# Performance work log

Hardware: AMD Instinct MI355X
Metric: run time of the kernel (lower is better)

## Reference

```python
import jax, jax.numpy as jnp
import numpy as np

B, T, C = 4, 2048, 768
H, KVH, D = 6, 6, 128
HALF = D // 2


def setup_inputs() -> dict:
    key = jax.random.key(0)
    ks = jax.random.split(key, 5)
    x = jax.random.normal(ks[0], (B, T, C), dtype=jnp.float32)
    # true rotary frequencies
    inv_freq = 1.0 / (10000.0 ** (jnp.arange(HALF, dtype=jnp.float32) / HALF))
    ang = jnp.arange(T, dtype=jnp.float32)[:, None] * inv_freq[None, :]  # [T, HALF]
    cos, sin = jnp.cos(ang), jnp.sin(ang)
    s = 0.02
    wq = jax.random.normal(ks[1], (H * D, C), dtype=jnp.float32) * s
    wk = jax.random.normal(ks[2], (KVH * D, C), dtype=jnp.float32) * s
    wv = jax.random.normal(ks[3], (KVH * D, C), dtype=jnp.float32) * s
    wproj = jax.random.normal(ks[4], (C, C), dtype=jnp.float32) * s
    return {"x": x, "cos": cos, "sin": sin, "wq": wq, "wk": wk, "wv": wv, "wproj": wproj}


def _norm(t, eps=1e-6):
    # torch: (x - mean) / (std + eps), std unbiased (ddof=1)
    mean = jnp.mean(t, axis=-1, keepdims=True)
    var = jnp.sum((t - mean) ** 2, axis=-1, keepdims=True) / (t.shape[-1] - 1)
    return (t - mean) / (jnp.sqrt(var) + eps)


def _rope(t, cos, sin):
    # t: [B, T, heads, D]; cos/sin: [T, HALF]
    x1, x2 = t[..., :HALF], t[..., HALF:]
    c = cos[None, :, None, :]
    s = sin[None, :, None, :]
    return jnp.concatenate([x1 * c + x2 * s, -x1 * s + x2 * c], axis=-1)


def reference(x, cos, sin, wq, wk, wv, wproj):
    q = jnp.einsum('btc,oc->bto', x, wq).reshape(B, T, H, D)
    k = jnp.einsum('btc,oc->bto', x, wk).reshape(B, T, KVH, D)
    v = jnp.einsum('btc,oc->bto', x, wv).reshape(B, T, KVH, D)
    q = _norm(_rope(q, cos, sin))
    k = _norm(_rope(k, cos, sin))
    # -> [B, heads, T, D]
    q = q.transpose(0, 2, 1, 3)
    k = k.transpose(0, 2, 1, 3)
    v = v.transpose(0, 2, 1, 3)
    # nrep = H // KVH == 1, repeat_kv is a no-op here
    scale = 1.0 / jnp.sqrt(jnp.float32(D))
    scores = jnp.einsum('bhtd,bhsd->bhts', q, k) * scale  # [B,H,T,T]
    causal = jnp.tril(jnp.ones((T, T), dtype=bool))
    scores = jnp.where(causal[None, None], scores, jnp.float32(-1e30))
    attn = jax.nn.softmax(scores, axis=-1)
    y = jnp.einsum('bhts,bhsd->bhtd', attn, v)
    y = y.transpose(0, 2, 1, 3).reshape(B, T, H * D)
    return jnp.einsum('bto,co->btc', y, wproj)
```

## Files before the change

### kernel.cpp

```cpp
#include <hip/hip_runtime.h>

#define BB 4
#define TT 2048
#define CC 768
#define HH 6
#define DD 128
#define BT (BB * TT)
#define HALF 64
#define NBH (BB * HH)
#define QKSCALE 0.12753785627919282f

typedef __bf16 v8bf __attribute__((ext_vector_type(8)));
typedef float f32x4 __attribute__((ext_vector_type(4)));

__device__ __forceinline__ unsigned short f2b(float f) {
  union { float f; unsigned u; } v; v.f = f;
  unsigned r = v.u + 0x7FFFu + ((v.u >> 16) & 1u);
  return (unsigned short)(r >> 16);
}
__device__ __forceinline__ float b2f(unsigned short u) {
  union { unsigned u; float f; } v; v.u = (unsigned)u << 16;
  return v.f;
}
__device__ __forceinline__ unsigned pk2(float f0, float f1) {
  union { float f; unsigned u; } a, b; a.f = f1; b.f = f0;
  return __builtin_amdgcn_perm(a.u, b.u, 0x07060302u);
}

__device__ __forceinline__ void load_lds16(const void* g, void* l) {
  __builtin_amdgcn_global_load_lds(
      (const __attribute__((address_space(1))) unsigned int*)g,
      (__attribute__((address_space(3))) unsigned int*)(unsigned int)(unsigned long long)(l),
      16, 0, 0);
}

__global__ __launch_bounds__(256) void cvt_all_kernel(const float* __restrict__ x,
                                                      const float* __restrict__ w0,
                                                      const float* __restrict__ w1,
                                                      const float* __restrict__ w2,
                                                      const float* __restrict__ w3,
                                                      unsigned short* __restrict__ xb,
                                                      unsigned short* __restrict__ wb) {
  int bx = blockIdx.x;
  const float* src;
  unsigned short* dst;
  int i;
  if (bx < 6144) {
    src = x; dst = xb; i = bx * 256 + threadIdx.x;
  } else {
    int bsel = (bx - 6144) / 576;
    src = bsel == 0 ? w0 : bsel == 1 ? w1 : bsel == 2 ? w2 : w3;
    dst = wb + bsel * 589824;
    i = ((bx - 6144) % 576) * 256 + threadIdx.x;
  }
  float4 f = ((const float4*)src)[i];
  ushort4 o;
  o.x = f2b(f.x); o.y = f2b(f.y); o.z = f2b(f.z); o.w = f2b(f.w);
  ((ushort4*)dst)[i] = o;
}

__global__ __launch_bounds__(256) void gemm_qkv(const unsigned short* __restrict__ A,
                                                const unsigned short* __restrict__ Wall,
                                                unsigned short* __restrict__ qb,
                                                unsigned short* __restrict__ kb,
                                                unsigned short* __restrict__ vt) {
  __shared__ __align__(16) unsigned short As[2][512 * 8];
  __shared__ __align__(16) unsigned short Bs[2][512 * 8];
  const int m0 = blockIdx.x * 128;
  const int wsel = blockIdx.y / HH, h = blockIdx.y % HH;
  const unsigned short* W = Wall + (size_t)wsel * 589824 + (size_t)h * 128 * CC;
  const int tid = threadIdx.x;
  const int wave = tid >> 6, lane = tid & 63;
  const int fr = lane & 15, quad = lane >> 4;
  const int wm = (wave & 1) * 64, wn = (wave >> 1) * 64;

  f32x4 acc[4][4];
#pragma unroll
  for (int i = 0; i < 4; i++)
#pragma unroll
    for (int j = 0; j < 4; j++) acc[i][j] = (f32x4){0.f, 0.f, 0.f, 0.f};

  auto stage = [&](int kk, int buf) {
#pragma unroll
    for (int it = 0; it < 2; it++) {
      int base_slot = wave * 128 + it * 64;
      int sigma = base_slot + lane;
      int r = sigma >> 2, g = (sigma & 3) ^ ((r >> 1) & 3);
      load_lds16(A + (size_t)(m0 + r) * CC + kk + g * 8, &As[buf][base_slot * 8]);
      load_lds16(W + (size_t)r * CC + kk + g * 8, &Bs[buf][base_slot * 8]);
    }
  };

  stage(0, 0);
  __syncthreads();
  for (int step = 0; step < CC / 32; step++) {
    int buf = step & 1;
    if (step + 1 < CC / 32) stage((step + 1) * 32, buf ^ 1);
    v8bf af[4], bfr[4];
#pragma unroll
    for (int i = 0; i < 4; i++) {
      int ra = wm + i * 16 + fr;
      af[i] = *(const v8bf*)&As[buf][(4 * ra + (quad ^ ((ra >> 1) & 3))) * 8];
      int rb = wn + i * 16 + fr;
      bfr[i] = *(const v8bf*)&Bs[buf][(4 * rb + (quad ^ ((rb >> 1) & 3))) * 8];
    }
#pragma unroll
    for (int i = 0; i < 4; i++)
#pragma unroll
      for (int j = 0; j < 4; j++)
        acc[i][j] = __builtin_amdgcn_mfma_f32_16x16x32_bf16(af[i], bfr[j], acc[i][j], 0, 0, 0);
    __syncthreads();
  }

  if (wsel < 2) {
    unsigned short* dst = wsel ? kb : qb;
#pragma unroll
    for (int i = 0; i < 4; i++) {
      int rr0 = m0 + wm + i * 16 + quad * 4;
      int b = rr0 >> 11, t0 = rr0 & 2047;
      size_t base = ((size_t)(b * HH + h) * TT + t0) * DD;
#pragma unroll
      for (int j = 0; j < 4; j++) {
        int d = wn + j * 16 + fr;
#pragma unroll
        for (int r = 0; r < 4; r++)
          dst[base + (size_t)r * DD + d] = f2b(acc[i][j][r]);
      }
    }
  } else {
#pragma unroll
    for (int i = 0; i < 4; i++) {
      int rr0 = m0 + wm + i * 16 + quad * 4;
      int b = rr0 >> 11, t0 = rr0 & 2047;
      int bh = b * HH + h;
#pragma unroll
      for (int j = 0; j < 4; j++) {
        int d = wn + j * 16 + fr;
        ushort4 u = { f2b(acc[i][j][0]), f2b(acc[i][j][1]),
                      f2b(acc[i][j][2]), f2b(acc[i][j][3]) };
        *(ushort4*)&vt[((size_t)bh * DD + d) * TT + t0] = u;
      }
    }
  }
}

__global__ __launch_bounds__(256) void gemm_w64(const unsigned short* __restrict__ A,
                                                const unsigned short* __restrict__ W,
                                                float* __restrict__ C) {
  __shared__ __align__(16) unsigned short As[2][256 * 8];
  __shared__ __align__(16) unsigned short Bs[2][512 * 8];
  const int m0 = blockIdx.x * 64, n0 = blockIdx.y * 128;
  const int tid = threadIdx.x;
  const int wave = tid >> 6, lane = tid & 63;
  const int fr = lane & 15, quad = lane >> 4;
  const int wm = (wave & 1) * 32, wn = (wave >> 1) * 64;

  f32x4 acc[2][4];
#pragma unroll
  for (int i = 0; i < 2; i++)
#pragma unroll
    for (int j = 0; j < 4; j++) acc[i][j] = (f32x4){0.f, 0.f, 0.f, 0.f};

  auto stage = [&](int kk, int buf) {
    {
      int base_slot = wave * 64;
      int sigma = base_slot + lane;
      int r = sigma >> 2, g = (sigma & 3) ^ ((r >> 1) & 3);
      load_lds16(A + (size_t)(m0 + r) * CC + kk + g * 8, &As[buf][base_slot * 8]);
    }
#pragma unroll
    for (int it = 0; it < 2; it++) {
      int base_slot = wave * 128 + it * 64;
      int sigma = base_slot + lane;
      int r = sigma >> 2, g = (sigma & 3) ^ ((r >> 1) & 3);
      load_lds16(W + (size_t)(n0 + r) * CC + kk + g * 8, &Bs[buf][base_slot * 8]);
    }
  };

  stage(0, 0);
  __syncthreads();
  for (int step = 0; step < CC / 32; step++) {
    int buf = step & 1;
    if (step + 1 < CC / 32) stage((step + 1) * 32, buf ^ 1);
    v8bf af[2], bfr[4];
#pragma unroll
    for (int i = 0; i < 2; i++) {
      int ra = wm + i * 16 + fr;
      af[i] = *(const v8bf*)&As[buf][(4 * ra + (quad ^ ((ra >> 1) & 3))) * 8];
    }
#pragma unroll
    for (int j = 0; j < 4; j++) {
      int rb = wn + j * 16 + fr;
      bfr[j] = *(const v8bf*)&Bs[buf][(4 * rb + (quad ^ ((rb >> 1) & 3))) * 8];
    }
#pragma unroll
    for (int i = 0; i < 2; i++)
#pragma unroll
      for (int j = 0; j < 4; j++)
        acc[i][j] = __builtin_amdgcn_mfma_f32_16x16x32_bf16(af[i], bfr[j], acc[i][j], 0, 0, 0);
    __syncthreads();
  }

  const int orow = m0 + wm + quad * 4;
#pragma unroll
  for (int i = 0; i < 2; i++)
#pragma unroll
    for (int j = 0; j < 4; j++) {
      int oc = n0 + wn + j * 16 + fr;
#pragma unroll
      for (int r = 0; r < 4; r++)
        C[(size_t)(orow + i * 16 + r) * CC + oc] = acc[i][j][r];
    }
}

__global__ __launch_bounds__(256) void rope_all_kernel(unsigned short* __restrict__ qb,
                                                       unsigned short* __restrict__ kb,
                                                       const float* __restrict__ cosb,
                                                       const float* __restrict__ sinb) {
  int bx = blockIdx.x;
  unsigned short* qk = (bx < 12288) ? qb : kb;
  float scale = (bx < 12288) ? QKSCALE : 1.0f;
  int idx = (bx % 12288) * 4 + (threadIdx.x >> 6);
  int lane = threadIdx.x & 63;
  int tpos = idx & (TT - 1);
  size_t base = (size_t)idx * DD;

  float x1 = b2f(qk[base + lane]);
  float x2 = b2f(qk[base + HALF + lane]);
  float c = cosb[tpos * HALF + lane];
  float s = sinb[tpos * HALF + lane];
  float o1 = x1 * c + x2 * s;
  float o2 = x2 * c - x1 * s;

  float sum = o1 + o2;
#pragma unroll
  for (int off = 32; off; off >>= 1) sum += __shfl_xor(sum, off);
  float mean = sum * (1.f / 128.f);
  float d1 = o1 - mean, d2 = o2 - mean;
  float vs = d1 * d1 + d2 * d2;
#pragma unroll
  for (int off = 32; off; off >>= 1) vs += __shfl_xor(vs, off);
  float inv = scale / (sqrtf(vs * (1.f / 127.f)) + 1e-6f);

  qk[base + lane] = f2b(d1 * inv);
  qk[base + HALF + lane] = f2b(d2 * inv);
}

__global__ __launch_bounds__(256, 4) void attn_mfma(const unsigned short* __restrict__ qtb,
                                                    const unsigned short* __restrict__ ktb,
                                                    const unsigned short* __restrict__ vtb,
                                                    unsigned short* __restrict__ Opart,
                                                    float* __restrict__ lpart) {
  __shared__ __align__(16) unsigned short Ks[2][512 * 8];
  __shared__ __align__(16) unsigned short Vts[2][512 * 8];

  const int u = blockIdx.x;
  const int bh = u % NBH;
  const int uu = u / NBH;
  int qt, c;
  if (uu < 16)      { qt = 15 - (uu >> 2); c = uu & 3; }
  else if (uu < 28) { int k = uu - 16; int q3 = k / 3; qt = 11 - q3; c = k - q3 * 3; }
  else if (uu < 36) { int k = uu - 28; qt = 7 - (k >> 1); c = k & 1; }
  else              { qt = 3 - (uu - 36); c = 0; }
  const int t0 = c * 16;
  const int t1 = min(t0 + 16, 4 * qt + 4);
  const int niter = t1 - t0;

  const int tid = threadIdx.x;
  const int wave = tid >> 6, lane = tid & 63;
  const int fr = lane & 15, quad = lane >> 4;
  const int idxf = 4 * ((quad & 1) * 32 + fr);
  const int idxs = idxf + 64;
  const size_t head_base = (size_t)bh * TT * DD;
  const int m0 = qt * 128 + wave * 32;

  v8bf qf[2][4];
#pragma unroll
  for (int qs = 0; qs < 2; qs++)
#pragma unroll
    for (int kbk = 0; kbk < 4; kbk++)
      qf[qs][kbk] = *(const v8bf*)(qtb + head_base +
                                   (size_t)(m0 + qs * 16 + fr) * DD + kbk * 32 + quad * 8);

  const __bf16 one_bf = (__bf16)1.0f;
  v8bf ones = {one_bf, one_bf, one_bf, one_bf, one_bf, one_bf, one_bf, one_bf};

  f32x4 oacc[2][8];
#pragma unroll
  for (int qs = 0; qs < 2; qs++)
#pragma unroll
    for (int i = 0; i < 8; i++) oacc[qs][i] = (f32x4){0.f, 0.f, 0.f, 0.f};
  f32x4 lacc[2] = {(f32x4){0.f, 0.f, 0.f, 0.f}, (f32x4){0.f, 0.f, 0.f, 0.f}};

  auto stage = [&](int jt, int buf) {
    const unsigned short* kbase = ktb + head_base + (size_t)(jt * 32) * DD;
    const unsigned short* vbase = vtb + head_base + jt * 32;
#pragma unroll
    for (int it = 0; it < 2; it++) {
      int base_slot = it * 256 + wave * 64;
      int sigma = base_slot + lane;
      int s = sigma >> 4, gk = (sigma & 15) ^ (s & 7);
      load_lds16(kbase + (size_t)s * DD + gk * 8, &Ks[buf][base_slot * 8]);
      int d = sigma >> 2, gv = (sigma & 3) ^ ((d >> 1) & 3);
      load_lds16(vbase + (size_t)d * TT + gv * 8, &Vts[buf][base_slot * 8]);
    }
  };

  stage(t0, 0);
  __syncthreads();

  for (int it = 0; it < niter; it++) {
    const int jt = t0 + it;
    const int buf = it & 1;
    if (it + 1 < niter) stage(jt + 1, buf ^ 1);

    const int j0 = jt * 32;
    if (j0 <= m0 + 31) {
      f32x4 st[2][2];
#pragma unroll
      for (int qs = 0; qs < 2; qs++) { st[qs][0] = (f32x4){0,0,0,0}; st[qs][1] = (f32x4){0,0,0,0}; }
      __builtin_amdgcn_s_setprio(1);
#pragma unroll
      for (int kbk = 0; kbk < 4; kbk++) {
        int g = 4 * kbk + quad;
        v8bf a0 = *(const v8bf*)&Ks[buf][(16 * fr + (g ^ (fr & 7))) * 8];
        v8bf a1 = *(const v8bf*)&Ks[buf][(16 * (fr + 16) + (g ^ (fr & 7))) * 8];
        st[0][0] = __builtin_amdgcn_mfma_f32_16x16x32_bf16(a0, qf[0][kbk], st[0][0], 0, 0, 0);
        st[0][1] = __builtin_amdgcn_mfma_f32_16x16x32_bf16(a1, qf[0][kbk], st[0][1], 0, 0, 0);
        st[1][0] = __builtin_amdgcn_mfma_f32_16x16x32_bf16(a0, qf[1][kbk], st[1][0], 0, 0, 0);
        st[1][1] = __builtin_amdgcn_mfma_f32_16x16x32_bf16(a1, qf[1][kbk], st[1][1], 0, 0, 0);
      }
      __builtin_amdgcn_s_setprio(0);

      const bool diag = (j0 + 31 > m0);
      v8bf pa0, pa1;
#pragma unroll
      for (int qs = 0; qs < 2; qs++) {
        float p[8];
        if (diag) {
          const int qrow = m0 + qs * 16 + fr;
#pragma unroll
          for (int r = 0; r < 4; r++) {
            int c0 = j0 + quad * 4 + r;
            p[r]     = (c0      <= qrow) ? exp2f(st[qs][0][r]) : 0.f;
            p[4 + r] = (c0 + 16 <= qrow) ? exp2f(st[qs][1][r]) : 0.f;
          }
        } else {
#pragma unroll
          for (int r = 0; r < 4; r++) { p[r] = exp2f(st[qs][0][r]); p[4 + r] = exp2f(st[qs][1][r]); }
        }
        unsigned A0 = pk2(p[0], p[1]), A1 = pk2(p[2], p[3]);
        unsigned B0 = pk2(p[4], p[5]), B1 = pk2(p[6], p[7]);
        unsigned alo0 = (unsigned)__builtin_amdgcn_ds_bpermute(idxf, (int)A0);
        unsigned alo1 = (unsigned)__builtin_amdgcn_ds_bpermute(idxf, (int)A1);
        unsigned ahi0 = (unsigned)__builtin_amdgcn_ds_bpermute(idxs, (int)A0);
        unsigned ahi1 = (unsigned)__builtin_amdgcn_ds_bpermute(idxs, (int)A1);
        unsigned blo0 = (unsigned)__builtin_amdgcn_ds_bpermute(idxf, (int)B0);
        unsigned blo1 = (unsigned)__builtin_amdgcn_ds_bpermute(idxf, (int)B1);
        unsigned bhi0 = (unsigned)__builtin_amdgcn_ds_bpermute(idxs, (int)B0);
        unsigned bhi1 = (unsigned)__builtin_amdgcn_ds_bpermute(idxs, (int)B1);
        const bool ql = (quad < 2);
        union { unsigned w[4]; v8bf v; } pa;
        pa.w[0] = ql ? alo0 : blo0;
        pa.w[1] = ql ? alo1 : blo1;
        pa.w[2] = ql ? ahi0 : bhi0;
        pa.w[3] = ql ? ahi1 : bhi1;
        if (qs == 0) pa0 = pa.v; else pa1 = pa.v;
      }

      __builtin_amdgcn_s_setprio(1);
#pragma unroll
      for (int nt2 = 0; nt2 < 8; nt2++) {
        int d = nt2 * 16 + fr;
        v8bf vb = *(const v8bf*)&Vts[buf][(4 * d + (quad ^ ((d >> 1) & 3))) * 8];
        oacc[0][nt2] = __builtin_amdgcn_mfma_f32_16x16x32_bf16(pa0, vb, oacc[0][nt2], 0, 0, 0);
        oacc[1][nt2] = __builtin_amdgcn_mfma_f32_16x16x32_bf16(pa1, vb, oacc[1][nt2], 0, 0, 0);
      }
      lacc[0] = __builtin_amdgcn_mfma_f32_16x16x32_bf16(pa0, ones, lacc[0], 0, 0, 0);
      lacc[1] = __builtin_amdgcn_mfma_f32_16x16x32_bf16(pa1, ones, lacc[1], 0, 0, 0);
      __builtin_amdgcn_s_setprio(0);
    }
    __syncthreads();
  }

  unsigned short* Oc = Opart + (size_t)c * (NBH * TT * DD) + head_base;
#pragma unroll
  for (int qs = 0; qs < 2; qs++) {
#pragma unroll
    for (int nt2 = 0; nt2 < 8; nt2++)
#pragma unroll
      for (int r = 0; r < 4; r++)
        Oc[(size_t)(m0 + qs * 16 + quad * 4 + r) * DD + nt2 * 16 + fr] = f2b(oacc[qs][nt2][r]);
    if (fr == 0) {
#pragma unroll
      for (int r = 0; r < 4; r++)
        lpart[c * (NBH * TT) + bh * TT + m0 + qs * 16 + quad * 4 + r] = lacc[qs][r];
    }
  }
}

__global__ __launch_bounds__(256) void combine_kernel(const unsigned short* __restrict__ Opart,
                                                      const float* __restrict__ lpart,
                                                      unsigned short* __restrict__ yb) {
  int idx = blockIdx.x * 256 + threadIdx.x;
  int row = idx >> 5;
  int dg = (idx & 31) * 4;
  int t = row & 2047;
  int qt = t >> 7;
  int nc = (4 * qt + 4 + 15) >> 4;

  float a0 = 0.f, a1 = 0.f, a2 = 0.f, a3 = 0.f, l = 0.f;
  for (int cchunk = 0; cchunk < nc; cchunk++) {
    ushort4 o = *(const ushort4*)&Opart[(size_t)cchunk * (NBH * TT * DD) + (size_t)row * DD + dg];
    a0 += b2f(o.x); a1 += b2f(o.y); a2 += b2f(o.z); a3 += b2f(o.w);
    l += lpart[cchunk * (NBH * TT) + row];
  }
  float linv = 1.f / l;
  int bh = row >> 11;
  int b = bh / HH, h = bh % HH;
  ushort4 uo = { f2b(a0 * linv), f2b(a1 * linv), f2b(a2 * linv), f2b(a3 * linv) };
  *(ushort4*)&yb[((size_t)(b * TT + t)) * CC + h * DD + dg] = uo;
}

extern "C" void kernel_launch(void* const* d_in, const int* in_sizes, int n_in,
                              void* d_out, int out_size, void* d_ws, size_t ws_size,
                              hipStream_t stream) {
  const float* x     = (const float*)d_in[0];
  const float* cosb  = (const float*)d_in[1];
  const float* sinb  = (const float*)d_in[2];
  const float* wq    = (const float*)d_in[3];
  const float* wk    = (const float*)d_in[4];
  const float* wv    = (const float*)d_in[5];
  const float* wproj = (const float*)d_in[6];
  float* out = (float*)d_out;

  char* w = (char*)d_ws;
  unsigned short* q_t   = (unsigned short*)(w);
  unsigned short* k_t   = (unsigned short*)(w + 12582912);
  unsigned short* v_t   = (unsigned short*)(w + 25165824);
  unsigned short* yb    = (unsigned short*)(w + 37748736);
  unsigned short* xb    = (unsigned short*)(w + 50331648);
  float*          lpart = (float*)(w + 50331648);
  unsigned short* wb    = (unsigned short*)(w + 62914560);
  unsigned short* Opart = (unsigned short*)(w + 67633152);

  cvt_all_kernel<<<8448, 256, 0, stream>>>(x, wq, wk, wv, wproj, xb, wb);

  gemm_qkv<<<dim3(BT / 128, 3 * HH), 256, 0, stream>>>(xb, wb, q_t, k_t, v_t);

  rope_all_kernel<<<24576, 256, 0, stream>>>(q_t, k_t, cosb, sinb);

  attn_mfma<<<960, 256, 0, stream>>>(q_t, k_t, v_t, Opart, lpart);
  combine_kernel<<<6144, 256, 0, stream>>>(Opart, lpart, yb);

  gemm_w64<<<dim3(BT / 64, CC / 128), 256, 0, stream>>>(yb, wb + 3 * 589824, out);
}
```

Baseline: 288.5 us.

## Double KV tile to 64 keys per iteration in MFMA attention kernel

Increases the per-iteration key/value tile from 32 to 64 keys, doubling LDS buffers and restructuring the staging swizzle, score MFMAs, masking, and PV accumulation for two k-slices. The aim is to halve the number of loop iterations and __syncthreads barriers per block and amortize per-iteration overhead. In exchange, LDS use doubles to 64KB and register pressure rises, and the min-4-blocks launch bound is dropped, which may lower occupancy. More work on the causal diagonal is also wasted because the masked tile is coarser.

```diff
diff --git a/kernel.cpp b/kernel.cpp
--- a/kernel.cpp
+++ b/kernel.cpp
@@ -246,13 +246,13 @@
   qk[base + HALF + lane] = f2b(d2 * inv);
 }
 
-__global__ __launch_bounds__(256, 4) void attn_mfma(const unsigned short* __restrict__ qtb,
-                                                    const unsigned short* __restrict__ ktb,
-                                                    const unsigned short* __restrict__ vtb,
-                                                    unsigned short* __restrict__ Opart,
-                                                    float* __restrict__ lpart) {
-  __shared__ __align__(16) unsigned short Ks[2][512 * 8];
-  __shared__ __align__(16) unsigned short Vts[2][512 * 8];
+__global__ __launch_bounds__(256) void attn_mfma(const unsigned short* __restrict__ qtb,
+                                                 const unsigned short* __restrict__ ktb,
+                                                 const unsigned short* __restrict__ vtb,
+                                                 unsigned short* __restrict__ Opart,
+                                                 float* __restrict__ lpart) {
+  __shared__ __align__(16) unsigned short Ks[2][1024 * 8];
+  __shared__ __align__(16) unsigned short Vts[2][1024 * 8];
 
   const int u = blockIdx.x;
   const int bh = u % NBH;
@@ -262,8 +262,8 @@
   else if (uu < 28) { int k = uu - 16; int q3 = k / 3; qt = 11 - q3; c = k - q3 * 3; }
   else if (uu < 36) { int k = uu - 28; qt = 7 - (k >> 1); c = k & 1; }
   else              { qt = 3 - (uu - 36); c = 0; }
-  const int t0 = c * 16;
-  const int t1 = min(t0 + 16, 4 * qt + 4);
+  const int t0 = c * 8;
+  const int t1 = min(t0 + 8, 2 * qt + 2);
   const int niter = t1 - t0;
 
   const int tid = threadIdx.x;
@@ -293,15 +293,15 @@
   f32x4 lacc[2] = {(f32x4){0.f, 0.f, 0.f, 0.f}, (f32x4){0.f, 0.f, 0.f, 0.f}};
 
   auto stage = [&](int jt, int buf) {
-    const unsigned short* kbase = ktb + head_base + (size_t)(jt * 32) * DD;
-    const unsigned short* vbase = vtb + head_base + jt * 32;
-#pragma unroll
-    for (int it = 0; it < 2; it++) {
+    const unsigned short* kbase = ktb + head_base + (size_t)(jt * 64) * DD;
+    const unsigned short* vbase = vtb + head_base + jt * 64;
+#pragma unroll
+    for (int it = 0; it < 4; it++) {
       int base_slot = it * 256 + wave * 64;
       int sigma = base_slot + lane;
       int s = sigma >> 4, gk = (sigma & 15) ^ (s & 7);
       load_lds16(kbase + (size_t)s * DD + gk * 8, &Ks[buf][base_slot * 8]);
-      int d = sigma >> 2, gv = (sigma & 3) ^ ((d >> 1) & 3);
+      int d = sigma >> 3, gv = (sigma & 7) ^ ((d >> 1) & 7);
       load_lds16(vbase + (size_t)d * TT + gv * 8, &Vts[buf][base_slot * 8]);
     }
   };
@@ -314,70 +314,89 @@
     const int buf = it & 1;
     if (it + 1 < niter) stage(jt + 1, buf ^ 1);
 
-    const int j0 = jt * 32;
+    const int j0 = jt * 64;
     if (j0 <= m0 + 31) {
-      f32x4 st[2][2];
-#pragma unroll
-      for (int qs = 0; qs < 2; qs++) { st[qs][0] = (f32x4){0,0,0,0}; st[qs][1] = (f32x4){0,0,0,0}; }
+      f32x4 st[2][4];
+#pragma unroll
+      for (int qs = 0; qs < 2; qs++)
+#pragma unroll
+        for (int sb = 0; sb < 4; sb++) st[qs][sb] = (f32x4){0.f, 0.f, 0.f, 0.f};
       __builtin_amdgcn_s_setprio(1);
 #pragma unroll
       for (int kbk = 0; kbk < 4; kbk++) {
         int g = 4 * kbk + quad;
-        v8bf a0 = *(const v8bf*)&Ks[buf][(16 * fr + (g ^ (fr & 7))) * 8];
-        v8bf a1 = *(const v8bf*)&Ks[buf][(16 * (fr + 16) + (g ^ (fr & 7))) * 8];
+        int gx = (g ^ (fr & 7)) * 8;
+        v8bf a0 = *(const v8bf*)&Ks[buf][(16 * fr) * 8 + gx];
+        v8bf a1 = *(const v8bf*)&Ks[buf][(16 * (fr + 16)) * 8 + gx];
+        v8bf a2 = *(const v8bf*)&Ks[buf][(16 * (fr + 32)) * 8 + gx];
+        v8bf a3 = *(const v8bf*)&Ks[buf][(16 * (fr + 48)) * 8 + gx];
         st[0][0] = __builtin_amdgcn_mfma_f32_16x16x32_bf16(a0, qf[0][kbk], st[0][0], 0, 0, 0);
         st[0][1] = __builtin_amdgcn_mfma_f32_16x16x32_bf16(a1, qf[0][kbk], st[0][1], 0, 0, 0);
+        st[0][2] = __builtin_amdgcn_mfma_f32_16x16x32_bf16(a2, qf[0][kbk], st[0][2], 0, 0, 0);
+        st[0][3] = __builtin_amdgcn_mfma_f32_16x16x32_bf16(a3, qf[0][kbk], st[0][3], 0, 0, 0);
         st[1][0] = __builtin_amdgcn_mfma_f32_16x16x32_bf16(a0, qf[1][kbk], st[1][0], 0, 0, 0);
         st[1][1] = __builtin_amdgcn_mfma_f32_16x16x32_bf16(a1, qf[1][kbk], st[1][1], 0, 0, 0);
+        st[1][2] = __builtin_amdgcn_mfma_f32_16x16x32_bf16(a2, qf[1][kbk], st[1][2], 0, 0, 0);
+        st[1][3] = __builtin_amdgcn_mfma_f32_16x16x32_bf16(a3, qf[1][kbk], st[1][3], 0, 0, 0);
       }
       __builtin_amdgcn_s_setprio(0);
 
-      const bool diag = (j0 + 31 > m0);
-      v8bf pa0, pa1;
+      const bool diag = (j0 + 63 > m0);
+      v8bf pa[2][2];
 #pragma unroll
       for (int qs = 0; qs < 2; qs++) {
-        float p[8];
+        float p[16];
         if (diag) {
           const int qrow = m0 + qs * 16 + fr;
 #pragma unroll
-          for (int r = 0; r < 4; r++) {
-            int c0 = j0 + quad * 4 + r;
-            p[r]     = (c0      <= qrow) ? exp2f(st[qs][0][r]) : 0.f;
-            p[4 + r] = (c0 + 16 <= qrow) ? exp2f(st[qs][1][r]) : 0.f;
-          }
+          for (int sb = 0; sb < 4; sb++)
+#pragma unroll
+            for (int r = 0; r < 4; r++) {
+              int c0 = j0 + sb * 16 + quad * 4 + r;
+              p[sb * 4 + r] = (c0 <= qrow) ? exp2f(st[qs][sb][r]) : 0.f;
+            }
         } else {
 #pragma unroll
-          for (int r = 0; r < 4; r++) { p[r] = exp2f(st[qs][0][r]); p[4 + r] = exp2f(st[qs][1][r]); }
+          for (int sb = 0; sb < 4; sb++)
+#pragma unroll
+            for (int r = 0; r < 4; r++) p[sb * 4 + r] = exp2f(st[qs][sb][r]);
         }
-        unsigned A0 = pk2(p[0], p[1]), A1 = pk2(p[2], p[3]);
-        unsigned B0 = pk2(p[4], p[5]), B1 = pk2(p[6], p[7]);
-        unsigned alo0 = (unsigned)__builtin_amdgcn_ds_bpermute(idxf, (int)A0);
-        unsigned alo1 = (unsigned)__builtin_amdgcn_ds_bpermute(idxf, (int)A1);
-        unsigned ahi0 = (unsigned)__builtin_amdgcn_ds_bpermute(idxs, (int)A0);
-        unsigned ahi1 = (unsigned)__builtin_amdgcn_ds_bpermute(idxs, (int)A1);
-        unsigned blo0 = (unsigned)__builtin_amdgcn_ds_bpermute(idxf, (int)B0);
-        unsigned blo1 = (unsigned)__builtin_amdgcn_ds_bpermute(idxf, (int)B1);
-        unsigned bhi0 = (unsigned)__builtin_amdgcn_ds_bpermute(idxs, (int)B0);
-        unsigned bhi1 = (unsigned)__builtin_amdgcn_ds_bpermute(idxs, (int)B1);
-        const bool ql = (quad < 2);
-        union { unsigned w[4]; v8bf v; } pa;
-        pa.w[0] = ql ? alo0 : blo0;
-        pa.w[1] = ql ? alo1 : blo1;
-        pa.w[2] = ql ? ahi0 : bhi0;
-        pa.w[3] = ql ? ahi1 : bhi1;
-        if (qs == 0) pa0 = pa.v; else pa1 = pa.v;
+#pragma unroll
+        for (int ks = 0; ks < 2; ks++) {
+          unsigned A0 = pk2(p[ks * 8 + 0], p[ks * 8 + 1]), A1 = pk2(p[ks * 8 + 2], p[ks * 8 + 3]);
+          unsigned B0 = pk2(p[ks * 8 + 4], p[ks * 8 + 5]), B1 = pk2(p[ks * 8 + 6], p[ks * 8 + 7]);
+          unsigned alo0 = (unsigned)__builtin_amdgcn_ds_bpermute(idxf, (int)A0);
+          unsigned alo1 = (unsigned)__builtin_amdgcn_ds_bpermute(idxf, (int)A1);
+          unsigned ahi0 = (unsigned)__builtin_amdgcn_ds_bpermute(idxs, (int)A0);
+          unsigned ahi1 = (unsigned)__builtin_amdgcn_ds_bpermute(idxs, (int)A1);
+          unsigned blo0 = (unsigned)__builtin_amdgcn_ds_bpermute(idxf, (int)B0);
+          unsigned blo1 = (unsigned)__builtin_amdgcn_ds_bpermute(idxf, (int)B1);
+          unsigned bhi0 = (unsigned)__builtin_amdgcn_ds_bpermute(idxs, (int)B0);
+          unsigned bhi1 = (unsigned)__builtin_amdgcn_ds_bpermute(idxs, (int)B1);
+          const bool ql = (quad < 2);
+          union { unsigned w[4]; v8bf v; } pw;
+          pw.w[0] = ql ? alo0 : blo0;
+          pw.w[1] = ql ? alo1 : blo1;
+          pw.w[2] = ql ? ahi0 : bhi0;
+          pw.w[3] = ql ? ahi1 : bhi1;
+          pa[qs][ks] = pw.v;
+        }
       }
 
       __builtin_amdgcn_s_setprio(1);
 #pragma unroll
-      for (int nt2 = 0; nt2 < 8; nt2++) {
-        int d = nt2 * 16 + fr;
-        v8bf vb = *(const v8bf*)&Vts[buf][(4 * d + (quad ^ ((d >> 1) & 3))) * 8];
-        oacc[0][nt2] = __builtin_amdgcn_mfma_f32_16x16x32_bf16(pa0, vb, oacc[0][nt2], 0, 0, 0);
-        oacc[1][nt2] = __builtin_amdgcn_mfma_f32_16x16x32_bf16(pa1, vb, oacc[1][nt2], 0, 0, 0);
+      for (int ks = 0; ks < 2; ks++) {
+#pragma unroll
+        for (int nt2 = 0; nt2 < 8; nt2++) {
+          int d = nt2 * 16 + fr;
+          int swz = (d >> 1) & 7;
+          v8bf vb = *(const v8bf*)&Vts[buf][(8 * d + ((quad + 4 * ks) ^ swz)) * 8];
+          oacc[0][nt2] = __builtin_amdgcn_mfma_f32_16x16x32_bf16(pa[0][ks], vb, oacc[0][nt2], 0, 0, 0);
+          oacc[1][nt2] = __builtin_amdgcn_mfma_f32_16x16x32_bf16(pa[1][ks], vb, oacc[1][nt2], 0, 0, 0);
+        }
+        lacc[0] = __builtin_amdgcn_mfma_f32_16x16x32_bf16(pa[0][ks], ones, lacc[0], 0, 0, 0);
+        lacc[1] = __builtin_amdgcn_mfma_f32_16x16x32_bf16(pa[1][ks], ones, lacc[1], 0, 0, 0);
       }
-      lacc[0] = __builtin_amdgcn_mfma_f32_16x16x32_bf16(pa0, ones, lacc[0], 0, 0, 0);
-      lacc[1] = __builtin_amdgcn_mfma_f32_16x16x32_bf16(pa1, ones, lacc[1], 0, 0, 0);
       __builtin_amdgcn_s_setprio(0);
     }
     __syncthreads();
```

After: 267.0 us. 7.5% less time.

## Halve attention query tile to 64 rows and rebalance block-to-chunk schedule

Applied to the files above, without the earlier changes.

The attention kernel now processes 64 query rows per block (16 per wave) instead of 128, which doubles the grid and uses a new longest-first mapping of blocks to key chunks. Each wave holds one Q fragment and one set of output accumulators, so register pressure drops and more blocks can be resident. The intent is better load balance and occupancy on the causal triangle. In exchange, every K/V tile staged into shared memory now feeds half as many query rows, which doubles K/V traffic and the staging and sync cost per unit of work.

```diff
diff --git a/kernel.cpp b/kernel.cpp
--- a/kernel.cpp
+++ b/kernel.cpp
@@ -246,24 +246,25 @@
   qk[base + HALF + lane] = f2b(d2 * inv);
 }
 
-__global__ __launch_bounds__(256, 4) void attn_mfma(const unsigned short* __restrict__ qtb,
-                                                    const unsigned short* __restrict__ ktb,
-                                                    const unsigned short* __restrict__ vtb,
-                                                    unsigned short* __restrict__ Opart,
-                                                    float* __restrict__ lpart) {
+__global__ __launch_bounds__(256) void attn_mfma(const unsigned short* __restrict__ qtb,
+                                                 const unsigned short* __restrict__ ktb,
+                                                 const unsigned short* __restrict__ vtb,
+                                                 unsigned short* __restrict__ Opart,
+                                                 float* __restrict__ lpart) {
   __shared__ __align__(16) unsigned short Ks[2][512 * 8];
   __shared__ __align__(16) unsigned short Vts[2][512 * 8];
 
   const int u = blockIdx.x;
   const int bh = u % NBH;
   const int uu = u / NBH;
-  int qt, c;
-  if (uu < 16)      { qt = 15 - (uu >> 2); c = uu & 3; }
-  else if (uu < 28) { int k = uu - 16; int q3 = k / 3; qt = 11 - q3; c = k - q3 * 3; }
-  else if (uu < 36) { int k = uu - 28; qt = 7 - (k >> 1); c = k & 1; }
-  else              { qt = 3 - (uu - 36); c = 0; }
+  int qb, c;
+  if (uu < 25)       { c = 0; qb = 31 - uu; }
+  else if (uu < 42)  { c = 1; qb = 31 - (uu - 25); }
+  else if (uu < 51)  { c = 2; qb = 31 - (uu - 42); }
+  else if (uu == 51) { c = 3; qb = 31; }
+  else { int uu2 = uu - 52; int sidx = uu2 >> 2; c = uu2 & 3; qb = 8 * c + 6 - sidx; }
   const int t0 = c * 16;
-  const int t1 = min(t0 + 16, 4 * qt + 4);
+  const int t1 = min(t0 + 16, 2 * qb + 2);
   const int niter = t1 - t0;
 
   const int tid = threadIdx.x;
@@ -272,25 +273,21 @@
   const int idxf = 4 * ((quad & 1) * 32 + fr);
   const int idxs = idxf + 64;
   const size_t head_base = (size_t)bh * TT * DD;
-  const int m0 = qt * 128 + wave * 32;
-
-  v8bf qf[2][4];
-#pragma unroll
-  for (int qs = 0; qs < 2; qs++)
-#pragma unroll
-    for (int kbk = 0; kbk < 4; kbk++)
-      qf[qs][kbk] = *(const v8bf*)(qtb + head_base +
-                                   (size_t)(m0 + qs * 16 + fr) * DD + kbk * 32 + quad * 8);
+  const int m0 = qb * 64 + wave * 16;
+
+  v8bf qf[4];
+#pragma unroll
+  for (int kbk = 0; kbk < 4; kbk++)
+    qf[kbk] = *(const v8bf*)(qtb + head_base +
+                             (size_t)(m0 + fr) * DD + kbk * 32 + quad * 8);
 
   const __bf16 one_bf = (__bf16)1.0f;
   v8bf ones = {one_bf, one_bf, one_bf, one_bf, one_bf, one_bf, one_bf, one_bf};
 
-  f32x4 oacc[2][8];
-#pragma unroll
-  for (int qs = 0; qs < 2; qs++)
-#pragma unroll
-    for (int i = 0; i < 8; i++) oacc[qs][i] = (f32x4){0.f, 0.f, 0.f, 0.f};
-  f32x4 lacc[2] = {(f32x4){0.f, 0.f, 0.f, 0.f}, (f32x4){0.f, 0.f, 0.f, 0.f}};
+  f32x4 oacc[8];
+#pragma unroll
+  for (int i = 0; i < 8; i++) oacc[i] = (f32x4){0.f, 0.f, 0.f, 0.f};
+  f32x4 lacc = (f32x4){0.f, 0.f, 0.f, 0.f};
 
   auto stage = [&](int jt, int buf) {
     const unsigned short* kbase = ktb + head_base + (size_t)(jt * 32) * DD;
@@ -315,69 +312,61 @@
     if (it + 1 < niter) stage(jt + 1, buf ^ 1);
 
     const int j0 = jt * 32;
-    if (j0 <= m0 + 31) {
-      f32x4 st[2][2];
-#pragma unroll
-      for (int qs = 0; qs < 2; qs++) { st[qs][0] = (f32x4){0,0,0,0}; st[qs][1] = (f32x4){0,0,0,0}; }
+    if (j0 <= m0 + 15) {
+      f32x4 st0 = (f32x4){0.f, 0.f, 0.f, 0.f};
+      f32x4 st1 = (f32x4){0.f, 0.f, 0.f, 0.f};
       __builtin_amdgcn_s_setprio(1);
 #pragma unroll
       for (int kbk = 0; kbk < 4; kbk++) {
         int g = 4 * kbk + quad;
-        v8bf a0 = *(const v8bf*)&Ks[buf][(16 * fr + (g ^ (fr & 7))) * 8];
-        v8bf a1 = *(const v8bf*)&Ks[buf][(16 * (fr + 16) + (g ^ (fr & 7))) * 8];
-        st[0][0] = __builtin_amdgcn_mfma_f32_16x16x32_bf16(a0, qf[0][kbk], st[0][0], 0, 0, 0);
-        st[0][1] = __builtin_amdgcn_mfma_f32_16x16x32_bf16(a1, qf[0][kbk], st[0][1], 0, 0, 0);
-        st[1][0] = __builtin_amdgcn_mfma_f32_16x16x32_bf16(a0, qf[1][kbk], st[1][0], 0, 0, 0);
-        st[1][1] = __builtin_amdgcn_mfma_f32_16x16x32_bf16(a1, qf[1][kbk], st[1][1], 0, 0, 0);
+        int gx = (g ^ (fr & 7)) * 8;
+        v8bf a0 = *(const v8bf*)&Ks[buf][(16 * fr) * 8 + gx];
+        v8bf a1 = *(const v8bf*)&Ks[buf][(16 * (fr + 16)) * 8 + gx];
+        st0 = __builtin_amdgcn_mfma_f32_16x16x32_bf16(a0, qf[kbk], st0, 0, 0, 0);
+        st1 = __builtin_amdgcn_mfma_f32_16x16x32_bf16(a1, qf[kbk], st1, 0, 0, 0);
       }
       __builtin_amdgcn_s_setprio(0);
 
       const bool diag = (j0 + 31 > m0);
-      v8bf pa0, pa1;
-#pragma unroll
-      for (int qs = 0; qs < 2; qs++) {
-        float p[8];
-        if (diag) {
-          const int qrow = m0 + qs * 16 + fr;
-#pragma unroll
-          for (int r = 0; r < 4; r++) {
-            int c0 = j0 + quad * 4 + r;
-            p[r]     = (c0      <= qrow) ? exp2f(st[qs][0][r]) : 0.f;
-            p[4 + r] = (c0 + 16 <= qrow) ? exp2f(st[qs][1][r]) : 0.f;
-          }
-        } else {
-#pragma unroll
-          for (int r = 0; r < 4; r++) { p[r] = exp2f(st[qs][0][r]); p[4 + r] = exp2f(st[qs][1][r]); }
+      float p[8];
+      if (diag) {
+        const int qrow = m0 + fr;
+#pragma unroll
+        for (int r = 0; r < 4; r++) {
+          int c0 = j0 + quad * 4 + r;
+          p[r]     = (c0      <= qrow) ? exp2f(st0[r]) : 0.f;
+          p[4 + r] = (c0 + 16 <= qrow) ? exp2f(st1[r]) : 0.f;
         }
-        unsigned A0 = pk2(p[0], p[1]), A1 = pk2(p[2], p[3]);
-        unsigned B0 = pk2(p[4], p[5]), B1 = pk2(p[6], p[7]);
-        unsigned alo0 = (unsigned)__builtin_amdgcn_ds_bpermute(idxf, (int)A0);
-        unsigned alo1 = (unsigned)__builtin_amdgcn_ds_bpermute(idxf, (int)A1);
-        unsigned ahi0 = (unsigned)__builtin_amdgcn_ds_bpermute(idxs, (int)A0);
-        unsigned ahi1 = (unsigned)__builtin_amdgcn_ds_bpermute(idxs, (int)A1);
-        unsigned blo0 = (unsigned)__builtin_amdgcn_ds_bpermute(idxf, (int)B0);
-        unsigned blo1 = (unsigned)__builtin_amdgcn_ds_bpermute(idxf, (int)B1);
-        unsigned bhi0 = (unsigned)__builtin_amdgcn_ds_bpermute(idxs, (int)B0);
-        unsigned bhi1 = (unsigned)__builtin_amdgcn_ds_bpermute(idxs, (int)B1);
-        const bool ql = (quad < 2);
-        union { unsigned w[4]; v8bf v; } pa;
-        pa.w[0] = ql ? alo0 : blo0;
-        pa.w[1] = ql ? alo1 : blo1;
-        pa.w[2] = ql ? ahi0 : bhi0;
-        pa.w[3] = ql ? ahi1 : bhi1;
-        if (qs == 0) pa0 = pa.v; else pa1 = pa.v;
+      } else {
+#pragma unroll
+        for (int r = 0; r < 4; r++) { p[r] = exp2f(st0[r]); p[4 + r] = exp2f(st1[r]); }
       }
+      unsigned A0 = pk2(p[0], p[1]), A1 = pk2(p[2], p[3]);
+      unsigned B0 = pk2(p[4], p[5]), B1 = pk2(p[6], p[7]);
+      unsigned alo0 = (unsigned)__builtin_amdgcn_ds_bpermute(idxf, (int)A0);
+      unsigned alo1 = (unsigned)__builtin_amdgcn_ds_bpermute(idxf, (int)A1);
+      unsigned ahi0 = (unsigned)__builtin_amdgcn_ds_bpermute(idxs, (int)A0);
+      unsigned ahi1 = (unsigned)__builtin_amdgcn_ds_bpermute(idxs, (int)A1);
+      unsigned blo0 = (unsigned)__builtin_amdgcn_ds_bpermute(idxf, (int)B0);
+      unsigned blo1 = (unsigned)__builtin_amdgcn_ds_bpermute(idxf, (int)B1);
+      unsigned bhi0 = (unsigned)__builtin_amdgcn_ds_bpermute(idxs, (int)B0);
+      unsigned bhi1 = (unsigned)__builtin_amdgcn_ds_bpermute(idxs, (int)B1);
+      const bool ql = (quad < 2);
+      union { unsigned w[4]; v8bf v; } pw;
+      pw.w[0] = ql ? alo0 : blo0;
+      pw.w[1] = ql ? alo1 : blo1;
+      pw.w[2] = ql ? ahi0 : bhi0;
+      pw.w[3] = ql ? ahi1 : bhi1;
+      v8bf pa = pw.v;
 
       __builtin_amdgcn_s_setprio(1);
 #pragma unroll
       for (int nt2 = 0; nt2 < 8; nt2++) {
         int d = nt2 * 16 + fr;
         v8bf vb = *(const v8bf*)&Vts[buf][(4 * d + (quad ^ ((d >> 1) & 3))) * 8];
-        oacc[0][nt2] = __builtin_amdgcn_mfma_f32_16x16x32_bf16(pa0, vb, oacc[0][nt2], 0, 0, 0);
-        oacc[1][nt2] = __builtin_amdgcn_mfma_f32_16x16x32_bf16(pa1, vb, oacc[1][nt2], 0, 0, 0);
+        oacc[nt2] = __builtin_amdgcn_mfma_f32_16x16x32_bf16(pa, vb, oacc[nt2], 0, 0, 0);
       }
-      lacc[0] = __builtin_amdgcn_mfma_f32_16x16x32_bf16(pa0, ones, lacc[0], 0, 0, 0);
-      lacc[1] = __builtin_amdgcn_mfma_f32_16x16x32_bf16(pa1, ones, lacc[1], 0, 0, 0);
+      lacc = __builtin_amdgcn_mfma_f32_16x16x32_bf16(pa, ones, lacc, 0, 0, 0);
       __builtin_amdgcn_s_setprio(0);
     }
     __syncthreads();
@@ -385,17 +374,14 @@
 
   unsigned short* Oc = Opart + (size_t)c * (NBH * TT * DD) + head_base;
 #pragma unroll
-  for (int qs = 0; qs < 2; qs++) {
-#pragma unroll
-    for (int nt2 = 0; nt2 < 8; nt2++)
-#pragma unroll
-      for (int r = 0; r < 4; r++)
-        Oc[(size_t)(m0 + qs * 16 + quad * 4 + r) * DD + nt2 * 16 + fr] = f2b(oacc[qs][nt2][r]);
-    if (fr == 0) {
-#pragma unroll
-      for (int r = 0; r < 4; r++)
-        lpart[c * (NBH * TT) + bh * TT + m0 + qs * 16 + quad * 4 + r] = lacc[qs][r];
-    }
+  for (int nt2 = 0; nt2 < 8; nt2++)
+#pragma unroll
+    for (int r = 0; r < 4; r++)
+      Oc[(size_t)(m0 + quad * 4 + r) * DD + nt2 * 16 + fr] = f2b(oacc[nt2][r]);
+  if (fr == 0) {
+#pragma unroll
+    for (int r = 0; r < 4; r++)
+      lpart[c * (NBH * TT) + bh * TT + m0 + quad * 4 + r] = lacc[r];
   }
 }
 
@@ -450,7 +436,7 @@
 
   rope_all_kernel<<<24576, 256, 0, stream>>>(q_t, k_t, cosb, sinb);
 
-  attn_mfma<<<960, 256, 0, stream>>>(q_t, k_t, v_t, Opart, lpart);
+  attn_mfma<<<1920, 256, 0, stream>>>(q_t, k_t, v_t, Opart, lpart);
   combine_kernel<<<6144, 256, 0, stream>>>(Opart, lpart, yb);
 
   gemm_w64<<<dim3(BT / 64, CC / 128), 256, 0, stream>>>(yb, wb + 3 * 589824, out);
```

Result: faster. 243.7 us (-15.5%).

## Pre-swizzle K and V into MFMA fragment layout and drop LDS staging in attention

Applied to the files above, without the earlier changes.

The rope kernel now writes normalized K into a new buffer laid out exactly as the attention MFMA operand fragments, and the QKV GEMM writes V in a matching fragment-tiled layout. The attention kernel then loads K and V fragments straight from global memory into registers, removing the LDS double buffer, global_load_lds staging and the per-tile __syncthreads. It also swaps exp2f for a raw v_exp_f32 and drops the occupancy hint from launch bounds. The trade-off is that every wave in a block re-reads the same K/V tile from global/L2 instead of sharing it through LDS, with no software prefetch, and register pressure grows.

```diff
diff --git a/kernel.cpp b/kernel.cpp
--- a/kernel.cpp
+++ b/kernel.cpp
@@ -25,6 +25,9 @@
 __device__ __forceinline__ unsigned pk2(float f0, float f1) {
   union { float f; unsigned u; } a, b; a.f = f1; b.f = f0;
   return __builtin_amdgcn_perm(a.u, b.u, 0x07060302u);
+}
+__device__ __forceinline__ float ex2(float x) {
+  float r; asm("v_exp_f32 %0, %1" : "=v"(r) : "v"(x)); return r;
 }
 
 __device__ __forceinline__ void load_lds16(const void* g, void* l) {
@@ -131,14 +134,19 @@
 #pragma unroll
     for (int i = 0; i < 4; i++) {
       int rr0 = m0 + wm + i * 16 + quad * 4;
-      int b = rr0 >> 11, t0 = rr0 & 2047;
+      int b = rr0 >> 11, t0_ = rr0 & 2047;
       int bh = b * HH + h;
+      int jt = t0_ >> 5;
+      int qv = (t0_ >> 3) & 3;
+      int jj = t0_ & 7;
 #pragma unroll
       for (int j = 0; j < 4; j++) {
         int d = wn + j * 16 + fr;
+        int lane_v = qv * 16 + (d & 15);
+        size_t off = ((size_t)(bh * 64 + jt) * 8 + (d >> 4)) * 512 + lane_v * 8 + jj;
         ushort4 u = { f2b(acc[i][j][0]), f2b(acc[i][j][1]),
                       f2b(acc[i][j][2]), f2b(acc[i][j][3]) };
-        *(ushort4*)&vt[((size_t)bh * DD + d) * TT + t0] = u;
+        *(ushort4*)&vt[off] = u;
       }
     }
   }
@@ -214,19 +222,21 @@
 }
 
 __global__ __launch_bounds__(256) void rope_all_kernel(unsigned short* __restrict__ qb,
-                                                       unsigned short* __restrict__ kb,
+                                                       const unsigned short* __restrict__ kb,
                                                        const float* __restrict__ cosb,
-                                                       const float* __restrict__ sinb) {
+                                                       const float* __restrict__ sinb,
+                                                       unsigned short* __restrict__ k2) {
   int bx = blockIdx.x;
-  unsigned short* qk = (bx < 12288) ? qb : kb;
-  float scale = (bx < 12288) ? QKSCALE : 1.0f;
+  bool isq = (bx < 12288);
+  const unsigned short* src = isq ? qb : kb;
+  float scale = isq ? QKSCALE : 1.0f;
   int idx = (bx % 12288) * 4 + (threadIdx.x >> 6);
   int lane = threadIdx.x & 63;
   int tpos = idx & (TT - 1);
   size_t base = (size_t)idx * DD;
 
-  float x1 = b2f(qk[base + lane]);
-  float x2 = b2f(qk[base + HALF + lane]);
+  float x1 = b2f(src[base + lane]);
+  float x2 = b2f(src[base + HALF + lane]);
   float c = cosb[tpos * HALF + lane];
   float s = sinb[tpos * HALF + lane];
   float o1 = x1 * c + x2 * s;
@@ -242,18 +252,25 @@
   for (int off = 32; off; off >>= 1) vs += __shfl_xor(vs, off);
   float inv = scale / (sqrtf(vs * (1.f / 127.f)) + 1e-6f);
 
-  qk[base + lane] = f2b(d1 * inv);
-  qk[base + HALF + lane] = f2b(d2 * inv);
-}
-
-__global__ __launch_bounds__(256, 4) void attn_mfma(const unsigned short* __restrict__ qtb,
-                                                    const unsigned short* __restrict__ ktb,
-                                                    const unsigned short* __restrict__ vtb,
-                                                    unsigned short* __restrict__ Opart,
-                                                    float* __restrict__ lpart) {
-  __shared__ __align__(16) unsigned short Ks[2][512 * 8];
-  __shared__ __align__(16) unsigned short Vts[2][512 * 8];
-
+  if (isq) {
+    qb[base + lane] = f2b(d1 * inv);
+    qb[base + HALF + lane] = f2b(d2 * inv);
+  } else {
+    int bh = idx >> 11, t = idx & 2047;
+    int jt = t >> 5, rr = t & 31;
+    int half = rr >> 4, frv = rr & 15;
+    int q5 = (lane >> 3) & 3, j = lane & 7, kb1 = lane >> 5;
+    size_t b2 = (size_t)bh * 262144 + (size_t)jt * 4096 + half * 512 + q5 * 128 + frv * 8 + j;
+    k2[b2 + (size_t)kb1 * 1024] = f2b(d1 * inv);
+    k2[b2 + (size_t)(kb1 + 2) * 1024] = f2b(d2 * inv);
+  }
+}
+
+__global__ __launch_bounds__(256) void attn_mfma(const unsigned short* __restrict__ qtb,
+                                                 const unsigned short* __restrict__ k2b,
+                                                 const unsigned short* __restrict__ v2b,
+                                                 unsigned short* __restrict__ Opart,
+                                                 float* __restrict__ lpart) {
   const int u = blockIdx.x;
   const int bh = u % NBH;
   const int uu = u / NBH;
@@ -274,6 +291,9 @@
   const size_t head_base = (size_t)bh * TT * DD;
   const int m0 = qt * 128 + wave * 32;
 
+  const unsigned short* k2h = k2b + (size_t)bh * 262144;
+  const unsigned short* v2h = v2b + (size_t)bh * 262144;
+
   v8bf qf[2][4];
 #pragma unroll
   for (int qs = 0; qs < 2; qs++)
@@ -292,95 +312,78 @@
     for (int i = 0; i < 8; i++) oacc[qs][i] = (f32x4){0.f, 0.f, 0.f, 0.f};
   f32x4 lacc[2] = {(f32x4){0.f, 0.f, 0.f, 0.f}, (f32x4){0.f, 0.f, 0.f, 0.f}};
 
-  auto stage = [&](int jt, int buf) {
-    const unsigned short* kbase = ktb + head_base + (size_t)(jt * 32) * DD;
-    const unsigned short* vbase = vtb + head_base + jt * 32;
-#pragma unroll
-    for (int it = 0; it < 2; it++) {
-      int base_slot = it * 256 + wave * 64;
-      int sigma = base_slot + lane;
-      int s = sigma >> 4, gk = (sigma & 15) ^ (s & 7);
-      load_lds16(kbase + (size_t)s * DD + gk * 8, &Ks[buf][base_slot * 8]);
-      int d = sigma >> 2, gv = (sigma & 3) ^ ((d >> 1) & 3);
-      load_lds16(vbase + (size_t)d * TT + gv * 8, &Vts[buf][base_slot * 8]);
-    }
-  };
-
-  stage(t0, 0);
-  __syncthreads();
-
   for (int it = 0; it < niter; it++) {
     const int jt = t0 + it;
-    const int buf = it & 1;
-    if (it + 1 < niter) stage(jt + 1, buf ^ 1);
-
     const int j0 = jt * 32;
-    if (j0 <= m0 + 31) {
-      f32x4 st[2][2];
-#pragma unroll
-      for (int qs = 0; qs < 2; qs++) { st[qs][0] = (f32x4){0,0,0,0}; st[qs][1] = (f32x4){0,0,0,0}; }
-      __builtin_amdgcn_s_setprio(1);
-#pragma unroll
-      for (int kbk = 0; kbk < 4; kbk++) {
-        int g = 4 * kbk + quad;
-        v8bf a0 = *(const v8bf*)&Ks[buf][(16 * fr + (g ^ (fr & 7))) * 8];
-        v8bf a1 = *(const v8bf*)&Ks[buf][(16 * (fr + 16) + (g ^ (fr & 7))) * 8];
-        st[0][0] = __builtin_amdgcn_mfma_f32_16x16x32_bf16(a0, qf[0][kbk], st[0][0], 0, 0, 0);
-        st[0][1] = __builtin_amdgcn_mfma_f32_16x16x32_bf16(a1, qf[0][kbk], st[0][1], 0, 0, 0);
-        st[1][0] = __builtin_amdgcn_mfma_f32_16x16x32_bf16(a0, qf[1][kbk], st[1][0], 0, 0, 0);
-        st[1][1] = __builtin_amdgcn_mfma_f32_16x16x32_bf16(a1, qf[1][kbk], st[1][1], 0, 0, 0);
+    if (j0 > m0 + 31) continue;
+
+    const unsigned short* kp = k2h + (size_t)jt * 4096 + lane * 8;
+    v8bf kf[8];
+#pragma unroll
+    for (int i = 0; i < 8; i++) kf[i] = *(const v8bf*)&kp[i * 512];
+    const unsigned short* vp = v2h + (size_t)jt * 4096 + lane * 8;
+    v8bf vf[8];
+#pragma unroll
+    for (int i = 0; i < 8; i++) vf[i] = *(const v8bf*)&vp[i * 512];
+
+    f32x4 st[2][2];
+#pragma unroll
+    for (int qs = 0; qs < 2; qs++) { st[qs][0] = (f32x4){0,0,0,0}; st[qs][1] = (f32x4){0,0,0,0}; }
+    __builtin_amdgcn_s_setprio(1);
+#pragma unroll
+    for (int kbk = 0; kbk < 4; kbk++) {
+      st[0][0] = __builtin_amdgcn_mfma_f32_16x16x32_bf16(kf[kbk * 2],     qf[0][kbk], st[0][0], 0, 0, 0);
+      st[0][1] = __builtin_amdgcn_mfma_f32_16x16x32_bf16(kf[kbk * 2 + 1], qf[0][kbk], st[0][1], 0, 0, 0);
+      st[1][0] = __builtin_amdgcn_mfma_f32_16x16x32_bf16(kf[kbk * 2],     qf[1][kbk], st[1][0], 0, 0, 0);
+      st[1][1] = __builtin_amdgcn_mfma_f32_16x16x32_bf16(kf[kbk * 2 + 1], qf[1][kbk], st[1][1], 0, 0, 0);
+    }
+    __builtin_amdgcn_s_setprio(0);
+
+    const bool diag = (j0 + 31 > m0);
+    v8bf pa0, pa1;
+#pragma unroll
+    for (int qs = 0; qs < 2; qs++) {
+      float p[8];
+      if (diag) {
+        const int qrow = m0 + qs * 16 + fr;
+#pragma unroll
+        for (int r = 0; r < 4; r++) {
+          int c0 = j0 + quad * 4 + r;
+          p[r]     = (c0      <= qrow) ? ex2(st[qs][0][r]) : 0.f;
+          p[4 + r] = (c0 + 16 <= qrow) ? ex2(st[qs][1][r]) : 0.f;
+        }
+      } else {
+#pragma unroll
+        for (int r = 0; r < 4; r++) { p[r] = ex2(st[qs][0][r]); p[4 + r] = ex2(st[qs][1][r]); }
       }
-      __builtin_amdgcn_s_setprio(0);
-
-      const bool diag = (j0 + 31 > m0);
-      v8bf pa0, pa1;
-#pragma unroll
-      for (int qs = 0; qs < 2; qs++) {
-        float p[8];
-        if (diag) {
-          const int qrow = m0 + qs * 16 + fr;
-#pragma unroll
-          for (int r = 0; r < 4; r++) {
-            int c0 = j0 + quad * 4 + r;
-            p[r]     = (c0      <= qrow) ? exp2f(st[qs][0][r]) : 0.f;
-            p[4 + r] = (c0 + 16 <= qrow) ? exp2f(st[qs][1][r]) : 0.f;
-          }
-        } else {
-#pragma unroll
-          for (int r = 0; r < 4; r++) { p[r] = exp2f(st[qs][0][r]); p[4 + r] = exp2f(st[qs][1][r]); }
-        }
-        unsigned A0 = pk2(p[0], p[1]), A1 = pk2(p[2], p[3]);
-        unsigned B0 = pk2(p[4], p[5]), B1 = pk2(p[6], p[7]);
-        unsigned alo0 = (unsigned)__builtin_amdgcn_ds_bpermute(idxf, (int)A0);
-        unsigned alo1 = (unsigned)__builtin_amdgcn_ds_bpermute(idxf, (int)A1);
-        unsigned ahi0 = (unsigned)__builtin_amdgcn_ds_bpermute(idxs, (int)A0);
-        unsigned ahi1 = (unsigned)__builtin_amdgcn_ds_bpermute(idxs, (int)A1);
-        unsigned blo0 = (unsigned)__builtin_amdgcn_ds_bpermute(idxf, (int)B0);
-        unsigned blo1 = (unsigned)__builtin_amdgcn_ds_bpermute(idxf, (int)B1);
-        unsigned bhi0 = (unsigned)__builtin_amdgcn_ds_bpermute(idxs, (int)B0);
-        unsigned bhi1 = (unsigned)__builtin_amdgcn_ds_bpermute(idxs, (int)B1);
-        const bool ql = (quad < 2);
-        union { unsigned w[4]; v8bf v; } pa;
-        pa.w[0] = ql ? alo0 : blo0;
-        pa.w[1] = ql ? alo1 : blo1;
-        pa.w[2] = ql ? ahi0 : bhi0;
-        pa.w[3] = ql ? ahi1 : bhi1;
-        if (qs == 0) pa0 = pa.v; else pa1 = pa.v;
-      }
-
-      __builtin_amdgcn_s_setprio(1);
-#pragma unroll
-      for (int nt2 = 0; nt2 < 8; nt2++) {
-        int d = nt2 * 16 + fr;
-        v8bf vb = *(const v8bf*)&Vts[buf][(4 * d + (quad ^ ((d >> 1) & 3))) * 8];
-        oacc[0][nt2] = __builtin_amdgcn_mfma_f32_16x16x32_bf16(pa0, vb, oacc[0][nt2], 0, 0, 0);
-        oacc[1][nt2] = __builtin_amdgcn_mfma_f32_16x16x32_bf16(pa1, vb, oacc[1][nt2], 0, 0, 0);
-      }
-      lacc[0] = __builtin_amdgcn_mfma_f32_16x16x32_bf16(pa0, ones, lacc[0], 0, 0, 0);
-      lacc[1] = __builtin_amdgcn_mfma_f32_16x16x32_bf16(pa1, ones, lacc[1], 0, 0, 0);
-      __builtin_amdgcn_s_setprio(0);
-    }
-    __syncthreads();
+      unsigned A0 = pk2(p[0], p[1]), A1 = pk2(p[2], p[3]);
+      unsigned B0 = pk2(p[4], p[5]), B1 = pk2(p[6], p[7]);
+      unsigned alo0 = (unsigned)__builtin_amdgcn_ds_bpermute(idxf, (int)A0);
+      unsigned alo1 = (unsigned)__builtin_amdgcn_ds_bpermute(idxf, (int)A1);
+      unsigned ahi0 = (unsigned)__builtin_amdgcn_ds_bpermute(idxs, (int)A0);
+      unsigned ahi1 = (unsigned)__builtin_amdgcn_ds_bpermute(idxs, (int)A1);
+      unsigned blo0 = (unsigned)__builtin_amdgcn_ds_bpermute(idxf, (int)B0);
+      unsigned blo1 = (unsigned)__builtin_amdgcn_ds_bpermute(idxf, (int)B1);
+      unsigned bhi0 = (unsigned)__builtin_amdgcn_ds_bpermute(idxs, (int)B0);
+      unsigned bhi1 = (unsigned)__builtin_amdgcn_ds_bpermute(idxs, (int)B1);
+      const bool ql = (quad < 2);
+      union { unsigned w[4]; v8bf v; } pw;
+      pw.w[0] = ql ? alo0 : blo0;
+      pw.w[1] = ql ? alo1 : blo1;
+      pw.w[2] = ql ? ahi0 : bhi0;
+      pw.w[3] = ql ? ahi1 : bhi1;
+      if (qs == 0) pa0 = pw.v; else pa1 = pw.v;
+    }
+
+    __builtin_amdgcn_s_setprio(1);
+#pragma unroll
+    for (int nt2 = 0; nt2 < 8; nt2++) {
+      oacc[0][nt2] = __builtin_amdgcn_mfma_f32_16x16x32_bf16(pa0, vf[nt2], oacc[0][nt2], 0, 0, 0);
+      oacc[1][nt2] = __builtin_amdgcn_mfma_f32_16x16x32_bf16(pa1, vf[nt2], oacc[1][nt2], 0, 0, 0);
+    }
+    lacc[0] = __builtin_amdgcn_mfma_f32_16x16x32_bf16(pa0, ones, lacc[0], 0, 0, 0);
+    lacc[1] = __builtin_amdgcn_mfma_f32_16x16x32_bf16(pa1, ones, lacc[1], 0, 0, 0);
+    __builtin_amdgcn_s_setprio(0);
   }
 
   unsigned short* Oc = Opart + (size_t)c * (NBH * TT * DD) + head_base;
@@ -437,10 +440,11 @@
   char* w = (char*)d_ws;
   unsigned short* q_t   = (unsigned short*)(w);
   unsigned short* k_t   = (unsigned short*)(w + 12582912);
+  float*          lpart = (float*)(w + 12582912);
   unsigned short* v_t   = (unsigned short*)(w + 25165824);
   unsigned short* yb    = (unsigned short*)(w + 37748736);
   unsigned short* xb    = (unsigned short*)(w + 50331648);
-  float*          lpart = (float*)(w + 50331648);
+  unsigned short* K2    = (unsigned short*)(w + 50331648);
   unsigned short* wb    = (unsigned short*)(w + 62914560);
   unsigned short* Opart = (unsigned short*)(w + 67633152);
 
@@ -448,9 +452,9 @@
 
   gemm_qkv<<<dim3(BT / 128, 3 * HH), 256, 0, stream>>>(xb, wb, q_t, k_t, v_t);
 
-  rope_all_kernel<<<24576, 256, 0, stream>>>(q_t, k_t, cosb, sinb);
-
-  attn_mfma<<<960, 256, 0, stream>>>(q_t, k_t, v_t, Opart, lpart);
+  rope_all_kernel<<<24576, 256, 0, stream>>>(q_t, k_t, cosb, sinb, K2);
+
+  attn_mfma<<<960, 256, 0, stream>>>(q_t, K2, v_t, Opart, lpart);
   combine_kernel<<<6144, 256, 0, stream>>>(Opart, lpart, yb);
 
   gemm_w64<<<dim3(BT / 64, CC / 128), 256, 0, stream>>>(yb, wb + 3 * 589824, out);
```

After: 232.4 us. 1.24x faster.
